# Performance work log

Measured on AMD Instinct MI355X. Metric: run time of the kernel, lower is better.

## Reference

```python
import jax, jax.numpy as jnp
import numpy as np

B, NTOK, NATOM = 2, 512, 16384
C_TOKEN, C_ATOM, C_PAIR, C_S = 384, 128, 16, 384
NQ, NK, H, NB = 32, 128, 4, 3
DH = C_ATOM // H
NW = NATOM // NQ


def _ln(x, g=None, b=None, eps=1e-5):
    mu = jnp.mean(x, -1, keepdims=True)
    var = jnp.mean((x - mu) ** 2, -1, keepdims=True)
    xn = (x - mu) * jax.lax.rsqrt(var + eps)
    if g is not None:
        xn = xn * g
    if b is not None:
        xn = xn + b
    return xn


def setup_inputs() -> dict:
    key = jax.random.key(0)
    ks = iter(jax.random.split(key, 64))
    def rn(shape, scale=1.0):
        return scale * jax.random.normal(next(ks), shape, jnp.float32)
    W = 0.02
    inp = {
        'a': rn((B, NTOK, C_TOKEN)),
        'r_l': rn((B, NATOM, 3)),
        'extra_feats': rn((B, NATOM, C_ATOM)),
        'p_lm': rn((B, NW, NQ, NK, C_PAIR)),
        'atom_mask': jnp.ones((B, NATOM), jnp.float32),
        'atom_to_token_idx': jnp.sort(jax.random.randint(next(ks), (B, NATOM), 0, NTOK, jnp.int32), axis=-1),
        # top-level params
        'Wa': rn((C_TOKEN, C_ATOM), W),
        'lnq_g': jnp.ones((C_ATOM,), jnp.float32),
        'lnq_b': jnp.zeros((C_ATOM,), jnp.float32),
        'Wout': rn((C_ATOM, 3), W),
        # per-block (stacked over NB) atom-transformer params
        'ag_w': rn((NB, C_S, C_ATOM), W), 'ag_b': jnp.zeros((NB, C_ATOM), jnp.float32),
        'ab_w': rn((NB, C_S, C_ATOM), W),
        'wq': rn((NB, C_ATOM, C_ATOM), W), 'bq': jnp.zeros((NB, C_ATOM), jnp.float32),
        'wk': rn((NB, C_ATOM, C_ATOM), W), 'wv': rn((NB, C_ATOM, C_ATOM), W),
        'pg': jnp.ones((NB, C_PAIR), jnp.float32), 'pb': jnp.zeros((NB, C_PAIR), jnp.float32),
        'wpb': rn((NB, C_PAIR, H), W),
        'wg': rn((NB, C_ATOM, C_ATOM), W), 'wo': rn((NB, C_ATOM, C_ATOM), W),
        'sk_w': rn((NB, C_S, C_ATOM), W), 'sk_b': jnp.full((NB, C_ATOM), -2.0, jnp.float32),
        'tg_w': rn((NB, C_S, C_ATOM), W), 'tg_b': jnp.zeros((NB, C_ATOM), jnp.float32),
        'tb_w': rn((NB, C_S, C_ATOM), W),
        'wt1': rn((NB, C_ATOM, 2 * C_ATOM), W), 'wt2': rn((NB, C_ATOM, 2 * C_ATOM), W),
        'wto': rn((NB, 2 * C_ATOM, C_ATOM), W),
        'tk_w': rn((NB, C_S, C_ATOM), W), 'tk_b': jnp.full((NB, C_ATOM), -2.0, jnp.float32),
    }
    return inp


def reference(a, r_l, extra_feats, p_lm, atom_mask, atom_to_token_idx,
              Wa, lnq_g, lnq_b, Wout,
              ag_w, ag_b, ab_w, wq, bq, wk, wv, pg, pb, wpb, wg, wo, sk_w, sk_b,
              tg_w, tg_b, tb_w, wt1, wt2, wto, tk_w, tk_b):
    # token -> atom broadcast
    q = a @ Wa                                                  # [B, NTOK, C_ATOM]
    q = jnp.take_along_axis(q, atom_to_token_idx[..., None], axis=1)  # [B, NATOM, C_ATOM]
    q = q + extra_feats
    am = atom_mask[..., None]
    q = q * am
    # conditioning signal: extra_feats zero-padded from C_ATOM to C_S (as in torch code)
    s = jnp.pad(extra_feats, ((0, 0), (0, 0), (0, C_S - C_ATOM)))
    sn = _ln(s)
    # sliding-window key indices: keys centered on each query window
    centers = jnp.arange(NW) * NQ + NQ // 2
    idx = (centers - NK // 2)[:, None] + jnp.arange(NK)          # [NW, NK]
    valid = ((idx >= 0) & (idx < NATOM)).astype(jnp.float32)
    idxc = jnp.clip(idx, 0, NATOM - 1)
    keymask = valid[None] * jnp.take(atom_mask, idxc, axis=1)    # [B, NW, NK]

    x = q
    inv_sqrt_dh = 1.0 / np.sqrt(DH)
    for i in range(NB):
        # --- attention with pair bias (AdaLN conditioned) ---
        xa = jax.nn.sigmoid(sn @ ag_w[i] + ag_b[i]) * _ln(x) + sn @ ab_w[i]
        qh = (xa @ wq[i] + bq[i]).reshape(B, NW, NQ, H, DH)
        kh = (xa @ wk[i]).reshape(B, NATOM, H, DH)
        vh = (xa @ wv[i]).reshape(B, NATOM, H, DH)
        kw = jnp.take(kh, idxc, axis=1)                          # [B, NW, NK, H, DH]
        vw = jnp.take(vh, idxc, axis=1)
        bias = _ln(p_lm, pg[i], pb[i]) @ wpb[i]                  # [B, NW, NQ, NK, H]
        scores = jnp.einsum('bwqhd,bwkhd->bwqkh', qh, kw) * inv_sqrt_dh + bias
        scores = jnp.where(keymask[:, :, None, :, None] > 0, scores, -1e9)
        attn = jax.nn.softmax(scores, axis=3)
        o = jnp.einsum('bwqkh,bwkhd->bwqhd', attn, vw).reshape(B, NATOM, C_ATOM)
        gate = jax.nn.sigmoid(xa @ wg[i])
        attn_out = (gate * o) @ wo[i]
        x = x + jax.nn.sigmoid(sn @ sk_w[i] + sk_b[i]) * attn_out
        # --- conditioned transition (SwiGLU) ---
        xt = jax.nn.sigmoid(sn @ tg_w[i] + tg_b[i]) * _ln(x) + sn @ tb_w[i]
        hsw = jax.nn.silu(xt @ wt1[i]) * (xt @ wt2[i])
        x = x + jax.nn.sigmoid(sn @ tk_w[i] + tk_b[i]) * (hsw @ wto[i])

    x = x * am
    r = _ln(x, lnq_g, lnq_b) @ Wout                              # [B, NATOM, 3]
    return r
```

## Files before the change

kernel.cpp:

```cpp
#include <hip/hip_runtime.h>
#include <hip/hip_bf16.h>

typedef __bf16 bf16;
typedef __bf16 bf16x8 __attribute__((ext_vector_type(8)));
typedef float f32x4 __attribute__((ext_vector_type(4)));

#define DEV static __device__ __forceinline__

#define BB 2
#define NTOK 512
#define NATOM 16384
#define CT 384
#define CA 128
#define CP 16
#define CS 384
#define NQ 32
#define NK 128
#define NH 4
#define DH 32
#define NWIN 512
#define MTOT (BB*NATOM)

DEV bf16x8 lds_ld8(const bf16* p){
  union { uint2 u[2]; bf16x8 v; } t;
  t.u[0] = *reinterpret_cast<const uint2*>(p);
  t.u[1] = *reinterpret_cast<const uint2*>(p + 4);
  return t.v;
}
DEV f32x4 mfma16(bf16x8 a, bf16x8 b, f32x4 c){
  return __builtin_amdgcn_mfma_f32_16x16x32_bf16(a, b, c, 0, 0, 0);
}
DEV float sigmoidf_(float x){ return 1.f/(1.f + __expf(-x)); }
DEV float red_sum64(float v){
  #pragma unroll
  for (int off = 1; off < 64; off <<= 1) v += __shfl_xor(v, off);
  return v;
}

DEV void stage_A64(const bf16* __restrict__ Ag, int ldA, int m0, int k0,
                   bf16 (*As)[72], int tid){
  #pragma unroll
  for (int i = 0; i < 2; i++){
    int c = tid + i*256;
    int row = c >> 3, off = (c & 7) * 8;
    uint4 d = *reinterpret_cast<const uint4*>(Ag + (size_t)(m0 + row)*ldA + k0 + off);
    uint2* dst = reinterpret_cast<uint2*>(&As[row][off]);
    dst[0] = make_uint2(d.x, d.y);
    dst[1] = make_uint2(d.z, d.w);
  }
}
DEV void stage_W64(const float* __restrict__ Wg, int ldW, int k0, int n0,
                   bf16 (*Ws)[72], int tid){
  #pragma unroll
  for (int i = 0; i < 4; i++){
    int c = tid + i*256;
    int row = c >> 4, off = (c & 15) * 4;
    float4 d = *reinterpret_cast<const float4*>(Wg + (size_t)(k0 + row)*ldW + n0 + off);
    Ws[off+0][row] = (bf16)d.x;
    Ws[off+1][row] = (bf16)d.y;
    Ws[off+2][row] = (bf16)d.z;
    Ws[off+3][row] = (bf16)d.w;
  }
}
DEV void mma64(const bf16 (*As)[72], const bf16 (*Ws)[72], int wave, int lane,
               f32x4 acc[2][2]){
  int wm = (wave >> 1) * 32, wn = (wave & 1) * 32;
  int l16 = lane & 15, q8 = (lane >> 4) * 8;
  #pragma unroll
  for (int ks = 0; ks < 2; ks++){
    bf16x8 a0 = lds_ld8(&As[wm + l16][ks*32 + q8]);
    bf16x8 a1 = lds_ld8(&As[wm + 16 + l16][ks*32 + q8]);
    bf16x8 b0 = lds_ld8(&Ws[wn + l16][ks*32 + q8]);
    bf16x8 b1 = lds_ld8(&Ws[wn + 16 + l16][ks*32 + q8]);
    acc[0][0] = mfma16(a0, b0, acc[0][0]);
    acc[0][1] = mfma16(a0, b1, acc[0][1]);
    acc[1][0] = mfma16(a1, b0, acc[1][0]);
    acc[1][1] = mfma16(a1, b1, acc[1][1]);
  }
}

__global__ __launch_bounds__(128) void token_gemm(const float* __restrict__ a,
    const float* __restrict__ Wa, float* __restrict__ aW){
  __shared__ float arow[CT];
  int row = blockIdx.x;
  for (int j = threadIdx.x; j < CT; j += 128) arow[j] = a[(size_t)row*CT + j];
  __syncthreads();
  int c = threadIdx.x;
  float s = 0.f;
  for (int j = 0; j < CT; j++) s += arow[j] * Wa[(size_t)j*CA + c];
  aW[(size_t)row*CA + c] = s;
}

__global__ __launch_bounds__(256) void build_x0(const float* __restrict__ aW,
    const float* __restrict__ ef, const float* __restrict__ amask,
    const int* __restrict__ a2t, float* __restrict__ x,
    bf16* __restrict__ snc, float* __restrict__ tval){
  int ga = blockIdx.x * 4 + (threadIdx.x >> 6);
  int lane = threadIdx.x & 63;
  int b = ga >> 14;
  int tok = a2t[ga];
  float2 av = *reinterpret_cast<const float2*>(aW + ((size_t)(b*NTOK + tok))*CA + lane*2);
  float2 ev = *reinterpret_cast<const float2*>(ef + (size_t)ga*CA + lane*2);
  float m = amask[ga];
  *reinterpret_cast<float2*>(x + (size_t)ga*CA + lane*2) =
      make_float2((av.x + ev.x)*m, (av.y + ev.y)*m);
  float s = red_sum64(ev.x + ev.y);
  float mu = s * (1.f/384.f);
  float d0 = ev.x - mu, d1 = ev.y - mu;
  float vs = red_sum64(d0*d0 + d1*d1);
  float var = (vs + 256.f*mu*mu) * (1.f/384.f);
  float rs = rsqrtf(var + 1e-5f);
  bf16* sp = snc + (size_t)ga*CA + lane*2;
  sp[0] = (bf16)(d0*rs); sp[1] = (bf16)(d1*rs);
  if (lane == 0) tval[ga] = -mu*rs;
}

__global__ __launch_bounds__(128) void colsums(const float* ag, const float* ab,
    const float* sk, const float* tg, const float* tb, const float* tk,
    float* __restrict__ cs){
  int mat = blockIdx.x;
  int i = mat / 6, t = mat % 6;
  const float* base = t==0?ag : t==1?ab : t==2?sk : t==3?tg : t==4?tb : tk;
  const float* W = base + (size_t)i*CS*CA;
  int c = threadIdx.x;
  float s = 0.f;
  for (int k = CA; k < CS; k++) s += W[(size_t)k*CA + c];
  cs[(size_t)mat*CA + c] = s;
}

__global__ __launch_bounds__(256) void cond_gemm(const bf16* __restrict__ snc,
    const float* __restrict__ tval,
    const float* ag, const float* ab, const float* sk,
    const float* tg, const float* tb, const float* tk,
    const float* agb, const float* skb, const float* tgb, const float* tkb,
    const float* __restrict__ cs, bf16* __restrict__ cond){
  __shared__ bf16 As[64][72];
  __shared__ bf16 Ws[64][72];
  int tid = threadIdx.x, wave = tid >> 6, lane = tid & 63;
  int m0 = blockIdx.x * 64, n0 = blockIdx.y * 64;
  int type = blockIdx.z;
  const float* W; const float* bias; int sig;
  switch (type){
    case 0:  W = ag; bias = agb;     sig = 1; break;
    case 1:  W = ab; bias = nullptr; sig = 0; break;
    case 2:  W = sk; bias = skb;     sig = 1; break;
    case 3:  W = tg; bias = tgb;     sig = 1; break;
    case 4:  W = tb; bias = nullptr; sig = 0; break;
    default: W = tk; bias = tkb;     sig = 1; break;
  }
  f32x4 z = {0.f,0.f,0.f,0.f};
  f32x4 acc[2][2] = {{z,z},{z,z}};
  for (int kt = 0; kt < CA; kt += 64){
    stage_A64(snc, CA, m0, kt, As, tid);
    stage_W64(W, CA, kt, n0, Ws, tid);
    __syncthreads();
    mma64(As, Ws, wave, lane, acc);
    __syncthreads();
  }
  int wm = (wave >> 1)*32, wn = (wave & 1)*32, l16 = lane & 15, quad = lane >> 4;
  const float* csrow = cs + (size_t)type*CA;
  bf16* outp = cond + (size_t)type*MTOT*CA;
  #pragma unroll
  for (int mt = 0; mt < 2; mt++)
  #pragma unroll
  for (int nt = 0; nt < 2; nt++)
  #pragma unroll
  for (int r = 0; r < 4; r++){
    int m = m0 + wm + mt*16 + quad*4 + r;
    int n = n0 + wn + nt*16 + l16;
    float v = acc[mt][nt][r] + tval[m]*csrow[n];
    if (bias) v += bias[n];
    if (sig)  v = sigmoidf_(v);
    outp[(size_t)m*CA + n] = (bf16)v;
  }
}

__global__ __launch_bounds__(256) void adaln_kernel(const float* __restrict__ x,
    const bf16* __restrict__ g, const bf16* __restrict__ bt, bf16* __restrict__ outp){
  int ga = blockIdx.x * 4 + (threadIdx.x >> 6);
  int lane = threadIdx.x & 63;
  float2 xv = *reinterpret_cast<const float2*>(x + (size_t)ga*CA + lane*2);
  float s = red_sum64(xv.x + xv.y);
  float mu = s * (1.f/128.f);
  float d0 = xv.x - mu, d1 = xv.y - mu;
  float vs = red_sum64(d0*d0 + d1*d1);
  float rs = rsqrtf(vs*(1.f/128.f) + 1e-5f);
  const bf16* gp = g  + (size_t)ga*CA + lane*2;
  const bf16* bp = bt + (size_t)ga*CA + lane*2;
  bf16* op = outp + (size_t)ga*CA + lane*2;
  op[0] = (bf16)((float)gp[0]*(d0*rs) + (float)bp[0]);
  op[1] = (bf16)((float)gp[1]*(d1*rs) + (float)bp[1]);
}

__global__ __launch_bounds__(256) void qkvg_gemm(const bf16* __restrict__ xa,
    const float* wq, const float* bq, const float* wk, const float* wv,
    const float* wg, bf16* __restrict__ outq){
  __shared__ bf16 As[64][72];
  __shared__ bf16 Ws[64][72];
  int tid = threadIdx.x, wave = tid >> 6, lane = tid & 63;
  int m0 = blockIdx.x * 64;
  int sel = blockIdx.y >> 1;
  int n0 = (blockIdx.y & 1) * 64;
  const float* W = sel==0 ? wq : sel==1 ? wk : sel==2 ? wv : wg;
  f32x4 z = {0.f,0.f,0.f,0.f};
  f32x4 acc[2][2] = {{z,z},{z,z}};
  for (int kt = 0; kt < CA; kt += 64){
    stage_A64(xa, CA, m0, kt, As, tid);
    stage_W64(W, CA, kt, n0, Ws, tid);
    __syncthreads();
    mma64(As, Ws, wave, lane, acc);
    __syncthreads();
  }
  int wm = (wave >> 1)*32, wn = (wave & 1)*32, l16 = lane & 15, quad = lane >> 4;
  #pragma unroll
  for (int mt = 0; mt < 2; mt++)
  #pragma unroll
  for (int nt = 0; nt < 2; nt++)
  #pragma unroll
  for (int r = 0; r < 4; r++){
    int m = m0 + wm + mt*16 + quad*4 + r;
    int n = n0 + wn + nt*16 + l16;
    float v = acc[mt][nt][r];
    if (sel == 0) v += bq[n];
    if (sel == 3) v = sigmoidf_(v);
    outq[(size_t)m*512 + sel*128 + n] = (bf16)v;
  }
}

__global__ __launch_bounds__(256) void attn_kernel(const bf16* __restrict__ qkvg,
    const float* __restrict__ p_lm, const float* __restrict__ amask,
    const float* __restrict__ pgv, const float* __restrict__ pbv,
    const float* __restrict__ wpbv, bf16* __restrict__ go){
  __shared__ bf16 Qs[32][136];
  __shared__ bf16 Ks[128][136];
  __shared__ bf16 Vts[128][136];
  __shared__ float kmask[128];
  int w = blockIdx.x, b = blockIdx.y;
  int tid = threadIdx.x;
  int wave = tid >> 6, lane = tid & 63, l16 = lane & 15, quad = lane >> 4;
  size_t abase = (size_t)b*NATOM + (size_t)w*NQ;
  int kstart = w*NQ + NQ/2 - NK/2;
  if (tid < 128){
    int pos = kstart + tid;
    kmask[tid] = (pos >= 0 && pos < NATOM) ? amask[(size_t)b*NATOM + pos] : 0.f;
  }
  #pragma unroll
  for (int i = 0; i < 2; i++){
    int c = tid + i*256;
    int row = c >> 4, off = (c & 15)*8;
    uint4 d = *reinterpret_cast<const uint4*>(qkvg + (abase + row)*512 + off);
    *reinterpret_cast<uint4*>(&Qs[row][off]) = d;
  }
  #pragma unroll
  for (int i = 0; i < 8; i++){
    int c = tid + i*256;
    int row = c >> 4, off = (c & 15)*8;
    int ka = kstart + row; ka = ka < 0 ? 0 : (ka > NATOM-1 ? NATOM-1 : ka);
    uint4 d = *reinterpret_cast<const uint4*>(qkvg + ((size_t)b*NATOM + ka)*512 + 128 + off);
    *reinterpret_cast<uint4*>(&Ks[row][off]) = d;
  }
  #pragma unroll
  for (int i = 0; i < 16; i++){
    int c = tid + i*256;
    int row = c >> 5, off = (c & 31)*4;
    int ka = kstart + row; ka = ka < 0 ? 0 : (ka > NATOM-1 ? NATOM-1 : ka);
    uint2 d = *reinterpret_cast<const uint2*>(qkvg + ((size_t)b*NATOM + ka)*512 + 256 + off);
    union { uint2 u; bf16 h[4]; } t; t.u = d;
    Vts[off+0][row] = t.h[0];
    Vts[off+1][row] = t.h[1];
    Vts[off+2][row] = t.h[2];
    Vts[off+3][row] = t.h[3];
  }
  __syncthreads();
  int h = wave;
  f32x4 z4 = {0.f,0.f,0.f,0.f};
  f32x4 sacc[2][8];
  #pragma unroll
  for (int mt = 0; mt < 2; mt++)
    #pragma unroll
    for (int nt = 0; nt < 8; nt++) sacc[mt][nt] = z4;
  {
    bf16x8 bfr[8];
    #pragma unroll
    for (int nt = 0; nt < 8; nt++) bfr[nt] = lds_ld8(&Ks[nt*16 + l16][h*32 + quad*8]);
    #pragma unroll
    for (int mt = 0; mt < 2; mt++){
      bf16x8 a = lds_ld8(&Qs[mt*16 + l16][h*32 + quad*8]);
      #pragma unroll
      for (int nt = 0; nt < 8; nt++) sacc[mt][nt] = mfma16(a, bfr[nt], sacc[mt][nt]);
    }
  }
  __syncthreads();
  f32x4 wj4[16]; f32x4 wsum4 = z4, cconst4 = z4;
  #pragma unroll
  for (int j = 0; j < 16; j++){
    f32x4 wp = { wpbv[j*4+0], wpbv[j*4+1], wpbv[j*4+2], wpbv[j*4+3] };
    wj4[j] = pgv[j] * wp;
    wsum4 += wj4[j];
    cconst4 += pbv[j] * wp;
  }
  size_t pbase = ((size_t)(b*NWIN + w)) * NQ * NK * CP;
  bf16* BiasBuf = &Ks[0][0];
  {
    #pragma unroll 4
    for (int t = 0; t < 16; t++){
      int pid = t*64 + lane;
      int q = pid >> 5;
      int k = wave*32 + (pid & 31);
      const float* pp = p_lm + pbase + ((size_t)q*NK + k)*CP;
      float4 p0 = *reinterpret_cast<const float4*>(pp);
      float4 p1 = *reinterpret_cast<const float4*>(pp + 4);
      float4 p2 = *reinterpret_cast<const float4*>(pp + 8);
      float4 p3 = *reinterpret_cast<const float4*>(pp + 12);
      float sm = p0.x+p0.y+p0.z+p0.w + p1.x+p1.y+p1.z+p1.w
               + p2.x+p2.y+p2.z+p2.w + p3.x+p3.y+p3.z+p3.w;
      float sq = p0.x*p0.x+p0.y*p0.y+p0.z*p0.z+p0.w*p0.w
               + p1.x*p1.x+p1.y*p1.y+p1.z*p1.z+p1.w*p1.w
               + p2.x*p2.x+p2.y*p2.y+p2.z*p2.z+p2.w*p2.w
               + p3.x*p3.x+p3.y*p3.y+p3.z*p3.z+p3.w*p3.w;
      f32x4 dw = z4;
      dw += p0.x*wj4[0];  dw += p0.y*wj4[1];  dw += p0.z*wj4[2];  dw += p0.w*wj4[3];
      dw += p1.x*wj4[4];  dw += p1.y*wj4[5];  dw += p1.z*wj4[6];  dw += p1.w*wj4[7];
      dw += p2.x*wj4[8];  dw += p2.y*wj4[9];  dw += p2.z*wj4[10]; dw += p2.w*wj4[11];
      dw += p3.x*wj4[12]; dw += p3.y*wj4[13]; dw += p3.z*wj4[14]; dw += p3.w*wj4[15];
      float mu = sm * (1.f/16.f);
      float var = fmaxf(sq*(1.f/16.f) - mu*mu, 0.f);
      float rsg = rsqrtf(var + 1e-5f);
      f32x4 bias4 = rsg*(dw - mu*wsum4) + cconst4;
      union { uint2 u; bf16 hh[4]; } tb;
      tb.hh[0] = (bf16)bias4.x; tb.hh[1] = (bf16)bias4.y;
      tb.hh[2] = (bf16)bias4.z; tb.hh[3] = (bf16)bias4.w;
      *reinterpret_cast<uint2*>(&BiasBuf[((size_t)q*NK + k)*4]) = tb.u;
    }
  }
  __syncthreads();
  const float invs = 0.17677669529663689f;
  #pragma unroll
  for (int mt = 0; mt < 2; mt++)
  #pragma unroll
  for (int r = 0; r < 4; r++){
    int q = mt*16 + quad*4 + r;
    #pragma unroll
    for (int nt = 0; nt < 8; nt++){
      int k = nt*16 + l16;
      float biasv = (float)BiasBuf[((size_t)q*NK + k)*4 + h];
      float sv = sacc[mt][nt][r]*invs + biasv;
      sacc[mt][nt][r] = (kmask[k] > 0.f) ? sv : -1e9f;
    }
  }
  float rinv[2][4];
  #pragma unroll
  for (int mt = 0; mt < 2; mt++)
  #pragma unroll
  for (int r = 0; r < 4; r++){
    float mx = -3.0e38f;
    #pragma unroll
    for (int nt = 0; nt < 8; nt++) mx = fmaxf(mx, sacc[mt][nt][r]);
    #pragma unroll
    for (int off = 1; off < 16; off <<= 1) mx = fmaxf(mx, __shfl_xor(mx, off));
    float ss = 0.f;
    #pragma unroll
    for (int nt = 0; nt < 8; nt++){
      float e = __expf(sacc[mt][nt][r] - mx);
      sacc[mt][nt][r] = e; ss += e;
    }
    #pragma unroll
    for (int off = 1; off < 16; off <<= 1) ss += __shfl_xor(ss, off);
    rinv[mt][r] = 1.f/ss;
  }
  __syncthreads();
  bf16 (*Ph)[136] = reinterpret_cast<bf16(*)[136]>(&Ks[h*32][0]);
  #pragma unroll
  for (int mt = 0; mt < 2; mt++)
  #pragma unroll
  for (int nt = 0; nt < 8; nt++)
  #pragma unroll
  for (int r = 0; r < 4; r++)
    Ph[mt*16 + quad*4 + r][nt*16 + l16] = (bf16)(sacc[mt][nt][r]*rinv[mt][r]);
  f32x4 oacc[2][2] = {{z4,z4},{z4,z4}};
  #pragma unroll
  for (int kt = 0; kt < 4; kt++){
    bf16x8 a0 = lds_ld8(&Ph[l16][kt*32 + quad*8]);
    bf16x8 a1 = lds_ld8(&Ph[16 + l16][kt*32 + quad*8]);
    bf16x8 b0 = lds_ld8(&Vts[h*32 + l16][kt*32 + quad*8]);
    bf16x8 b1 = lds_ld8(&Vts[h*32 + 16 + l16][kt*32 + quad*8]);
    oacc[0][0] = mfma16(a0, b0, oacc[0][0]);
    oacc[0][1] = mfma16(a0, b1, oacc[0][1]);
    oacc[1][0] = mfma16(a1, b0, oacc[1][0]);
    oacc[1][1] = mfma16(a1, b1, oacc[1][1]);
  }
  #pragma unroll
  for (int mt = 0; mt < 2; mt++)
  #pragma unroll
  for (int nt = 0; nt < 2; nt++)
  #pragma unroll
  for (int r = 0; r < 4; r++){
    int q = mt*16 + quad*4 + r;
    int dcol = h*32 + nt*16 + l16;
    size_t arow = abase + q;
    float gate = (float)qkvg[arow*512 + 384 + dcol];
    go[arow*CA + dcol] = (bf16)(gate * oacc[mt][nt][r]);
  }
}

template<int K>
__global__ __launch_bounds__(256) void resid_gemm(const bf16* __restrict__ Ain,
    const float* __restrict__ W, const bf16* __restrict__ gatec,
    float* __restrict__ x){
  __shared__ bf16 As[64][72];
  __shared__ bf16 Ws[64][72];
  int tid = threadIdx.x, wave = tid >> 6, lane = tid & 63;
  int m0 = blockIdx.x * 64, n0 = blockIdx.y * 64;
  f32x4 z = {0.f,0.f,0.f,0.f};
  f32x4 acc[2][2] = {{z,z},{z,z}};
  for (int kt = 0; kt < K; kt += 64){
    stage_A64(Ain, K, m0, kt, As, tid);
    stage_W64(W, CA, kt, n0, Ws, tid);
    __syncthreads();
    mma64(As, Ws, wave, lane, acc);
    __syncthreads();
  }
  int wm = (wave >> 1)*32, wn = (wave & 1)*32, l16 = lane & 15, quad = lane >> 4;
  #pragma unroll
  for (int mt = 0; mt < 2; mt++)
  #pragma unroll
  for (int nt = 0; nt < 2; nt++)
  #pragma unroll
  for (int r = 0; r < 4; r++){
    int m = m0 + wm + mt*16 + quad*4 + r;
    int n = n0 + wn + nt*16 + l16;
    size_t idx = (size_t)m*CA + n;
    x[idx] += (float)gatec[idx] * acc[mt][nt][r];
  }
}

__global__ __launch_bounds__(256) void t12_gemm(const bf16* __restrict__ xt,
    const float* __restrict__ w1, const float* __restrict__ w2,
    bf16* __restrict__ hsw){
  __shared__ bf16 As[64][72];
  __shared__ bf16 Ws[64][72];
  int tid = threadIdx.x, wave = tid >> 6, lane = tid & 63;
  int m0 = blockIdx.x * 64, n0 = blockIdx.y * 64;
  f32x4 z = {0.f,0.f,0.f,0.f};
  f32x4 acc1[2][2] = {{z,z},{z,z}};
  f32x4 acc2[2][2] = {{z,z},{z,z}};
  for (int kt = 0; kt < CA; kt += 64){
    stage_A64(xt, CA, m0, kt, As, tid);
    stage_W64(w1, 2*CA, kt, n0, Ws, tid);
    __syncthreads();
    mma64(As, Ws, wave, lane, acc1);
    __syncthreads();
    stage_W64(w2, 2*CA, kt, n0, Ws, tid);
    __syncthreads();
    mma64(As, Ws, wave, lane, acc2);
    __syncthreads();
  }
  int wm = (wave >> 1)*32, wn = (wave & 1)*32, l16 = lane & 15, quad = lane >> 4;
  #pragma unroll
  for (int mt = 0; mt < 2; mt++)
  #pragma unroll
  for (int nt = 0; nt < 2; nt++)
  #pragma unroll
  for (int r = 0; r < 4; r++){
    int m = m0 + wm + mt*16 + quad*4 + r;
    int n = n0 + wn + nt*16 + l16;
    float v1 = acc1[mt][nt][r];
    float v2 = acc2[mt][nt][r];
    hsw[(size_t)m*(2*CA) + n] = (bf16)(v1*sigmoidf_(v1)*v2);
  }
}

__global__ __launch_bounds__(256) void final_kernel(const float* __restrict__ x,
    const float* __restrict__ amask, const float* __restrict__ lg,
    const float* __restrict__ lb, const float* __restrict__ Wout,
    float* __restrict__ outp){
  int ga = blockIdx.x * 4 + (threadIdx.x >> 6);
  int lane = threadIdx.x & 63;
  float2 xv = *reinterpret_cast<const float2*>(x + (size_t)ga*CA + lane*2);
  float m = amask[ga];
  xv.x *= m; xv.y *= m;
  float s = red_sum64(xv.x + xv.y);
  float mu = s * (1.f/128.f);
  float d0 = xv.x - mu, d1 = xv.y - mu;
  float vs = red_sum64(d0*d0 + d1*d1);
  float rs = rsqrtf(vs*(1.f/128.f) + 1e-5f);
  int c = lane*2;
  float xn0 = d0*rs*lg[c]   + lb[c];
  float xn1 = d1*rs*lg[c+1] + lb[c+1];
  float p0 = xn0*Wout[c*3+0] + xn1*Wout[(c+1)*3+0];
  float p1 = xn0*Wout[c*3+1] + xn1*Wout[(c+1)*3+1];
  float p2 = xn0*Wout[c*3+2] + xn1*Wout[(c+1)*3+2];
  p0 = red_sum64(p0); p1 = red_sum64(p1); p2 = red_sum64(p2);
  if (lane == 0){
    outp[(size_t)ga*3 + 0] = p0;
    outp[(size_t)ga*3 + 1] = p1;
    outp[(size_t)ga*3 + 2] = p2;
  }
}

extern "C" void kernel_launch(void* const* d_in, const int* in_sizes, int n_in,
                              void* d_out, int out_size, void* d_ws, size_t ws_size,
                              hipStream_t stream){
  (void)in_sizes; (void)n_in; (void)out_size; (void)ws_size;
  const float* a     = (const float*)d_in[0];
  const float* ef    = (const float*)d_in[2];
  const float* p_lm  = (const float*)d_in[3];
  const float* amask = (const float*)d_in[4];
  const int*   a2t   = (const int*)d_in[5];
  const float* Wa    = (const float*)d_in[6];
  const float* lnq_g = (const float*)d_in[7];
  const float* lnq_b = (const float*)d_in[8];
  const float* Wout  = (const float*)d_in[9];
  const float* ag_w  = (const float*)d_in[10];
  const float* ag_b  = (const float*)d_in[11];
  const float* ab_w  = (const float*)d_in[12];
  const float* wq    = (const float*)d_in[13];
  const float* bq    = (const float*)d_in[14];
  const float* wk    = (const float*)d_in[15];
  const float* wv    = (const float*)d_in[16];
  const float* pg    = (const float*)d_in[17];
  const float* pb    = (const float*)d_in[18];
  const float* wpb   = (const float*)d_in[19];
  const float* wg    = (const float*)d_in[20];
  const float* wo    = (const float*)d_in[21];
  const float* sk_w  = (const float*)d_in[22];
  const float* sk_b  = (const float*)d_in[23];
  const float* tg_w  = (const float*)d_in[24];
  const float* tg_b  = (const float*)d_in[25];
  const float* tb_w  = (const float*)d_in[26];
  const float* wt1   = (const float*)d_in[27];
  const float* wt2   = (const float*)d_in[28];
  const float* wto   = (const float*)d_in[29];
  const float* tk_w  = (const float*)d_in[30];
  const float* tk_b  = (const float*)d_in[31];
  float* out = (float*)d_out;
  char* ws = (char*)d_ws;

  const size_t OFF_X    = 0;
  const size_t OFF_SNC  = OFF_X    + (size_t)MTOT*CA*4;
  const size_t OFF_TVAL = OFF_SNC  + (size_t)MTOT*CA*2;
  const size_t OFF_AW   = OFF_TVAL + (size_t)MTOT*4;
  const size_t OFF_CS   = OFF_AW   + (size_t)BB*NTOK*CA*4;
  const size_t OFF_COND = OFF_CS   + 18*CA*4 + 256;
  const size_t OFF_XA   = OFF_COND + (size_t)6*MTOT*CA*2;
  const size_t OFF_QKVG = OFF_XA   + (size_t)MTOT*CA*2;
  const size_t OFF_GO   = OFF_QKVG + (size_t)MTOT*512*2;

  float* x    = (float*)(ws + OFF_X);
  bf16*  snc  = (bf16*)(ws + OFF_SNC);
  float* tval = (float*)(ws + OFF_TVAL);
  float* aW   = (float*)(ws + OFF_AW);
  float* cs   = (float*)(ws + OFF_CS);
  bf16*  cond = (bf16*)(ws + OFF_COND);
  bf16*  xa   = (bf16*)(ws + OFF_XA);
  bf16*  qkvg = (bf16*)(ws + OFF_QKVG);
  bf16*  go   = (bf16*)(ws + OFF_GO);
  const size_t CSZ = (size_t)MTOT*CA;

  token_gemm<<<BB*NTOK, 128, 0, stream>>>(a, Wa, aW);
  build_x0<<<MTOT/4, 256, 0, stream>>>(aW, ef, amask, a2t, x, snc, tval);
  colsums<<<18, 128, 0, stream>>>(ag_w, ab_w, sk_w, tg_w, tb_w, tk_w, cs);

  for (int i = 0; i < 3; i++){
    size_t o384 = (size_t)i*CS*CA, o128 = (size_t)i*CA*CA, ob = (size_t)i*CA;
    cond_gemm<<<dim3(MTOT/64, 2, 6), 256, 0, stream>>>(snc, tval,
        ag_w + o384, ab_w + o384, sk_w + o384, tg_w + o384, tb_w + o384, tk_w + o384,
        ag_b + ob, sk_b + ob, tg_b + ob, tk_b + ob,
        cs + (size_t)i*6*CA, cond);
    adaln_kernel<<<MTOT/4, 256, 0, stream>>>(x, cond + 0*CSZ, cond + 1*CSZ, xa);
    qkvg_gemm<<<dim3(MTOT/64, 8), 256, 0, stream>>>(xa,
        wq + o128, bq + ob, wk + o128, wv + o128, wg + o128, qkvg);
    attn_kernel<<<dim3(NWIN, BB), 256, 0, stream>>>(qkvg, p_lm, amask,
        pg + (size_t)i*CP, pb + (size_t)i*CP, wpb + (size_t)i*CP*NH, go);
    resid_gemm<128><<<dim3(MTOT/64, 2), 256, 0, stream>>>(go, wo + o128,
        cond + 2*CSZ, x);
    adaln_kernel<<<MTOT/4, 256, 0, stream>>>(x, cond + 3*CSZ, cond + 4*CSZ, xa);
    t12_gemm<<<dim3(MTOT/64, 4), 256, 0, stream>>>(xa,
        wt1 + (size_t)i*CA*2*CA, wt2 + (size_t)i*CA*2*CA, qkvg );
    resid_gemm<256><<<dim3(MTOT/64, 2), 256, 0, stream>>>(qkvg ,
        wto + (size_t)i*2*CA*CA, cond + 5*CSZ, x);
  }
  final_kernel<<<MTOT/4, 256, 0, stream>>>(x, amask, lnq_g, lnq_b, Wout, out);
}
```

Measured before the change: 1.125 ms.

## Pre-convert weights to bf16, hoist bias/cond GEMMs, fuse residual with adaLN

Adds a one-time kernel that converts and transposes all weight matrices to bf16 [N][K] layout. The GEMMs then read A and B fragments straight from global memory into MFMA registers, with no LDS staging and no per-block fp32 conversion. The conditioning GEMMs for all three blocks run in one launch, and the pair-bias LayerNorm projection for all blocks is computed once up front and stored in bf16. The residual GEMMs now also apply the next adaLN, and the 1/sqrt(dh) scale is folded into Q. In exchange there are larger workspace buffers (18 cond tensors plus a precomputed bias tensor) and more global-memory traffic for B fragments with no LDS reuse.

```diff
diff --git a/kernel.cpp b/kernel.cpp
--- a/kernel.cpp
+++ b/kernel.cpp
@@ -20,6 +20,15 @@
 #define DH 32
 #define NWIN 512
 #define MTOT (BB*NATOM)
+#define CSZ ((size_t)MTOT*CA)
+
+#define WT_COND_OFF 0
+#define WT_QKVG_OFF 294912
+#define WT_WO_OFF   491520
+#define WT_T12_OFF  540672
+#define WT_WTO_OFF  737280
+#define WT_TOTAL    835584
+#define BIAS_I      16777216
 
 DEV bf16x8 lds_ld8(const bf16* p){
   union { uint2 u[2]; bf16x8 v; } t;
@@ -27,6 +36,11 @@
   t.u[1] = *reinterpret_cast<const uint2*>(p + 4);
   return t.v;
 }
+DEV bf16x8 ldg8(const bf16* p){
+  union { uint4 u; bf16x8 v; } t;
+  t.u = *reinterpret_cast<const uint4*>(p);
+  return t.v;
+}
 DEV f32x4 mfma16(bf16x8 a, bf16x8 b, f32x4 c){
   return __builtin_amdgcn_mfma_f32_16x16x32_bf16(a, b, c, 0, 0, 0);
 }
@@ -37,45 +51,46 @@
   return v;
 }
 
-DEV void stage_A64(const bf16* __restrict__ Ag, int ldA, int m0, int k0,
-                   bf16 (*As)[72], int tid){
-  #pragma unroll
-  for (int i = 0; i < 2; i++){
-    int c = tid + i*256;
-    int row = c >> 3, off = (c & 7) * 8;
-    uint4 d = *reinterpret_cast<const uint4*>(Ag + (size_t)(m0 + row)*ldA + k0 + off);
-    uint2* dst = reinterpret_cast<uint2*>(&As[row][off]);
-    dst[0] = make_uint2(d.x, d.y);
-    dst[1] = make_uint2(d.z, d.w);
-  }
-}
-DEV void stage_W64(const float* __restrict__ Wg, int ldW, int k0, int n0,
-                   bf16 (*Ws)[72], int tid){
-  #pragma unroll
-  for (int i = 0; i < 4; i++){
-    int c = tid + i*256;
-    int row = c >> 4, off = (c & 15) * 4;
-    float4 d = *reinterpret_cast<const float4*>(Wg + (size_t)(k0 + row)*ldW + n0 + off);
-    Ws[off+0][row] = (bf16)d.x;
-    Ws[off+1][row] = (bf16)d.y;
-    Ws[off+2][row] = (bf16)d.z;
-    Ws[off+3][row] = (bf16)d.w;
-  }
-}
-DEV void mma64(const bf16 (*As)[72], const bf16 (*Ws)[72], int wave, int lane,
-               f32x4 acc[2][2]){
-  int wm = (wave >> 1) * 32, wn = (wave & 1) * 32;
-  int l16 = lane & 15, q8 = (lane >> 4) * 8;
-  #pragma unroll
-  for (int ks = 0; ks < 2; ks++){
-    bf16x8 a0 = lds_ld8(&As[wm + l16][ks*32 + q8]);
-    bf16x8 a1 = lds_ld8(&As[wm + 16 + l16][ks*32 + q8]);
-    bf16x8 b0 = lds_ld8(&Ws[wn + l16][ks*32 + q8]);
-    bf16x8 b1 = lds_ld8(&Ws[wn + 16 + l16][ks*32 + q8]);
-    acc[0][0] = mfma16(a0, b0, acc[0][0]);
-    acc[0][1] = mfma16(a0, b1, acc[0][1]);
-    acc[1][0] = mfma16(a1, b0, acc[1][0]);
-    acc[1][1] = mfma16(a1, b1, acc[1][1]);
+__global__ __launch_bounds__(256) void wconv(
+    const float* ag, const float* ab, const float* sk,
+    const float* tg, const float* tb, const float* tk,
+    const float* wq, const float* wk, const float* wv, const float* wg,
+    const float* wo, const float* wt1, const float* wt2, const float* wto,
+    bf16* __restrict__ wt){
+  __shared__ __align__(16) bf16 T[64][264];
+  int s = blockIdx.x;
+  int mat, nslab;
+  if (s < 66){ mat = s >> 1; nslab = s & 1; }
+  else if (s < 90){ mat = 33 + (s-66)/4; nslab = (s-66)&3; }
+  else { mat = 39 + ((s-90)>>1); nslab = (s-90)&1; }
+  const float* src; int K, N; size_t dst;
+  if (mat < 18){ int i = mat/6, t = mat - i*6;
+    const float* base = t==0?ag:t==1?ab:t==2?sk:t==3?tg:t==4?tb:tk;
+    src = base + (size_t)i*CS*CA; K=128; N=128; dst = WT_COND_OFF + (size_t)mat*16384; }
+  else if (mat < 30){ int q = mat-18; int i=q>>2, sx=q&3;
+    const float* base = sx==0?wq:sx==1?wk:sx==2?wv:wg;
+    src = base + (size_t)i*16384; K=128; N=128; dst = WT_QKVG_OFF + (size_t)q*16384; }
+  else if (mat < 33){ src = wo + (size_t)(mat-30)*16384; K=128; N=128;
+    dst = WT_WO_OFF + (size_t)(mat-30)*16384; }
+  else if (mat < 39){ int q = mat-33; int i=q>>1, sx=q&1;
+    src = (sx? wt2 : wt1) + (size_t)i*32768; K=128; N=256;
+    dst = WT_T12_OFF + (size_t)q*32768; }
+  else { src = wto + (size_t)(mat-39)*32768; K=256; N=128;
+    dst = WT_WTO_OFF + (size_t)(mat-39)*32768; }
+  int n0 = nslab*64;
+  int tid = threadIdx.x;
+  for (int c = tid; c < K*16; c += 256){
+    int k = c >> 4, nq = c & 15;
+    float4 v = *reinterpret_cast<const float4*>(src + (size_t)k*N + n0 + nq*4);
+    T[nq*4+0][k] = (bf16)v.x; T[nq*4+1][k] = (bf16)v.y;
+    T[nq*4+2][k] = (bf16)v.z; T[nq*4+3][k] = (bf16)v.w;
+  }
+  __syncthreads();
+  int KQ = K >> 3;
+  for (int c = tid; c < 64*KQ; c += 256){
+    int n = c / KQ, kq = c - n*KQ;
+    uint4 d = *reinterpret_cast<const uint4*>(&T[n][kq*8]);
+    *reinterpret_cast<uint4*>(wt + dst + (size_t)(n0+n)*K + kq*8) = d;
   }
 }
 
@@ -128,50 +143,112 @@
   cs[(size_t)mat*CA + c] = s;
 }
 
-__global__ __launch_bounds__(256) void cond_gemm(const bf16* __restrict__ snc,
-    const float* __restrict__ tval,
-    const float* ag, const float* ab, const float* sk,
-    const float* tg, const float* tb, const float* tk,
-    const float* agb, const float* skb, const float* tgb, const float* tkb,
+__global__ __launch_bounds__(256) void cond_all(const bf16* __restrict__ snc,
+    const float* __restrict__ tval, const bf16* __restrict__ wtc,
+    const float* __restrict__ ag_b, const float* __restrict__ sk_b,
+    const float* __restrict__ tg_b, const float* __restrict__ tk_b,
     const float* __restrict__ cs, bf16* __restrict__ cond){
-  __shared__ bf16 As[64][72];
-  __shared__ bf16 Ws[64][72];
   int tid = threadIdx.x, wave = tid >> 6, lane = tid & 63;
-  int m0 = blockIdx.x * 64, n0 = blockIdx.y * 64;
-  int type = blockIdx.z;
-  const float* W; const float* bias; int sig;
-  switch (type){
-    case 0:  W = ag; bias = agb;     sig = 1; break;
-    case 1:  W = ab; bias = nullptr; sig = 0; break;
-    case 2:  W = sk; bias = skb;     sig = 1; break;
-    case 3:  W = tg; bias = tgb;     sig = 1; break;
-    case 4:  W = tb; bias = nullptr; sig = 0; break;
-    default: W = tk; bias = tkb;     sig = 1; break;
-  }
-  f32x4 z = {0.f,0.f,0.f,0.f};
-  f32x4 acc[2][2] = {{z,z},{z,z}};
-  for (int kt = 0; kt < CA; kt += 64){
-    stage_A64(snc, CA, m0, kt, As, tid);
-    stage_W64(W, CA, kt, n0, Ws, tid);
-    __syncthreads();
-    mma64(As, Ws, wave, lane, acc);
-    __syncthreads();
-  }
-  int wm = (wave >> 1)*32, wn = (wave & 1)*32, l16 = lane & 15, quad = lane >> 4;
-  const float* csrow = cs + (size_t)type*CA;
-  bf16* outp = cond + (size_t)type*MTOT*CA;
-  #pragma unroll
-  for (int mt = 0; mt < 2; mt++)
-  #pragma unroll
-  for (int nt = 0; nt < 2; nt++)
-  #pragma unroll
-  for (int r = 0; r < 4; r++){
-    int m = m0 + wm + mt*16 + quad*4 + r;
-    int n = n0 + wn + nt*16 + l16;
-    float v = acc[mt][nt][r] + tval[m]*csrow[n];
-    if (bias) v += bias[n];
-    if (sig)  v = sigmoidf_(v);
-    outp[(size_t)m*CA + n] = (bf16)v;
+  int l16 = lane & 15, quad = lane >> 4;
+  int m0 = blockIdx.x*64; int i = blockIdx.y;
+  const bf16* Ar = snc + (size_t)(m0 + wave*16 + l16)*CA;
+  bf16x8 a[4];
+  #pragma unroll
+  for (int ks = 0; ks < 4; ks++) a[ks] = ldg8(Ar + ks*32 + quad*8);
+  float tv[4];
+  #pragma unroll
+  for (int r = 0; r < 4; r++) tv[r] = tval[m0 + wave*16 + quad*4 + r];
+  for (int t = 0; t < 6; t++){
+    const bf16* Wt = wtc + (size_t)(i*6+t)*16384;
+    const float* csr = cs + (size_t)(i*6+t)*CA;
+    const float* bias = t==0 ? ag_b + (size_t)i*CA : t==2 ? sk_b + (size_t)i*CA
+                      : t==3 ? tg_b + (size_t)i*CA : t==5 ? tk_b + (size_t)i*CA : nullptr;
+    bool sig = (t==0)||(t==2)||(t==3)||(t==5);
+    f32x4 z = {0.f,0.f,0.f,0.f};
+    f32x4 acc[8];
+    #pragma unroll
+    for (int nt = 0; nt < 8; nt++) acc[nt] = z;
+    #pragma unroll
+    for (int nt = 0; nt < 8; nt++){
+      const bf16* Bp = Wt + (size_t)(nt*16 + l16)*128 + quad*8;
+      #pragma unroll
+      for (int ks = 0; ks < 4; ks++)
+        acc[nt] = mfma16(a[ks], ldg8(Bp + ks*32), acc[nt]);
+    }
+    bf16* op = cond + (size_t)(i*6+t)*CSZ;
+    #pragma unroll
+    for (int nt = 0; nt < 8; nt++)
+    #pragma unroll
+    for (int r = 0; r < 4; r++){
+      int m = m0 + wave*16 + quad*4 + r;
+      int n = nt*16 + l16;
+      float v = acc[nt][r] + tv[r]*csr[n];
+      if (bias) v += bias[n];
+      if (sig)  v = sigmoidf_(v);
+      op[(size_t)m*CA + n] = (bf16)v;
+    }
+  }
+}
+
+__global__ __launch_bounds__(256) void bias_all(const float* __restrict__ p_lm,
+    const float* __restrict__ pg, const float* __restrict__ pb,
+    const float* __restrict__ wpb, bf16* __restrict__ biasg){
+  __shared__ f32x4 wjS[3][16];
+  __shared__ f32x4 extraS[3][2];
+  int w = blockIdx.x, b = blockIdx.y;
+  int tid = threadIdx.x;
+  if (tid < 48){
+    int i = tid >> 4, j = tid & 15;
+    f32x4 wp = *reinterpret_cast<const f32x4*>(wpb + (size_t)(i*16+j)*4);
+    wjS[i][j] = pg[i*16+j]*wp;
+  }
+  __syncthreads();
+  if (tid < 3){
+    f32x4 s = {0.f,0.f,0.f,0.f}, c = {0.f,0.f,0.f,0.f};
+    for (int j = 0; j < 16; j++){
+      s += wjS[tid][j];
+      f32x4 wp = *reinterpret_cast<const f32x4*>(wpb + (size_t)(tid*16+j)*4);
+      c += pb[tid*16+j]*wp;
+    }
+    extraS[tid][0] = s; extraS[tid][1] = c;
+  }
+  __syncthreads();
+  size_t pbase = (size_t)(b*NWIN + w)*(NQ*NK*CP);
+  size_t obase = (size_t)(b*NWIN + w)*4096*4;
+  for (int i = 0; i < 3; i++){
+    f32x4 wj[16];
+    #pragma unroll
+    for (int j = 0; j < 16; j++) wj[j] = wjS[i][j];
+    f32x4 wsum = extraS[i][0], cc = extraS[i][1];
+    bf16* ob = biasg + (size_t)i*BIAS_I + obase;
+    #pragma unroll 2
+    for (int t = 0; t < 16; t++){
+      int pid = t*256 + tid;
+      const float* pp = p_lm + pbase + (size_t)pid*16;
+      float4 p0 = *reinterpret_cast<const float4*>(pp);
+      float4 p1 = *reinterpret_cast<const float4*>(pp + 4);
+      float4 p2 = *reinterpret_cast<const float4*>(pp + 8);
+      float4 p3 = *reinterpret_cast<const float4*>(pp + 12);
+      float sm = p0.x+p0.y+p0.z+p0.w + p1.x+p1.y+p1.z+p1.w
+               + p2.x+p2.y+p2.z+p2.w + p3.x+p3.y+p3.z+p3.w;
+      float sq = p0.x*p0.x+p0.y*p0.y+p0.z*p0.z+p0.w*p0.w
+               + p1.x*p1.x+p1.y*p1.y+p1.z*p1.z+p1.w*p1.w
+               + p2.x*p2.x+p2.y*p2.y+p2.z*p2.z+p2.w*p2.w
+               + p3.x*p3.x+p3.y*p3.y+p3.z*p3.z+p3.w*p3.w;
+      f32x4 dw = {0.f,0.f,0.f,0.f};
+      dw += p0.x*wj[0];  dw += p0.y*wj[1];  dw += p0.z*wj[2];  dw += p0.w*wj[3];
+      dw += p1.x*wj[4];  dw += p1.y*wj[5];  dw += p1.z*wj[6];  dw += p1.w*wj[7];
+      dw += p2.x*wj[8];  dw += p2.y*wj[9];  dw += p2.z*wj[10]; dw += p2.w*wj[11];
+      dw += p3.x*wj[12]; dw += p3.y*wj[13]; dw += p3.z*wj[14]; dw += p3.w*wj[15];
+      float mu = sm * (1.f/16.f);
+      float var = fmaxf(sq*(1.f/16.f) - mu*mu, 0.f);
+      float rsg = rsqrtf(var + 1e-5f);
+      f32x4 b4 = rsg*(dw - mu*wsum) + cc;
+      union { uint2 u; bf16 hh[4]; } tb;
+      tb.hh[0] = (bf16)b4.x; tb.hh[1] = (bf16)b4.y;
+      tb.hh[2] = (bf16)b4.z; tb.hh[3] = (bf16)b4.w;
+      *reinterpret_cast<uint2*>(ob + (size_t)pid*4) = tb.u;
+    }
   }
 }
 
@@ -193,44 +270,45 @@
 }
 
 __global__ __launch_bounds__(256) void qkvg_gemm(const bf16* __restrict__ xa,
-    const float* wq, const float* bq, const float* wk, const float* wv,
-    const float* wg, bf16* __restrict__ outq){
-  __shared__ bf16 As[64][72];
-  __shared__ bf16 Ws[64][72];
+    const bf16* __restrict__ wt, const float* __restrict__ bq,
+    bf16* __restrict__ outq){
   int tid = threadIdx.x, wave = tid >> 6, lane = tid & 63;
-  int m0 = blockIdx.x * 64;
-  int sel = blockIdx.y >> 1;
-  int n0 = (blockIdx.y & 1) * 64;
-  const float* W = sel==0 ? wq : sel==1 ? wk : sel==2 ? wv : wg;
+  int l16 = lane & 15, quad = lane >> 4;
+  int m0 = blockIdx.x*64;
+  int sel = blockIdx.y;
+  const bf16* Wt = wt + (size_t)sel*16384;
+  const bf16* Ar = xa + (size_t)(m0 + wave*16 + l16)*CA;
+  bf16x8 a[4];
+  #pragma unroll
+  for (int ks = 0; ks < 4; ks++) a[ks] = ldg8(Ar + ks*32 + quad*8);
   f32x4 z = {0.f,0.f,0.f,0.f};
-  f32x4 acc[2][2] = {{z,z},{z,z}};
-  for (int kt = 0; kt < CA; kt += 64){
-    stage_A64(xa, CA, m0, kt, As, tid);
-    stage_W64(W, CA, kt, n0, Ws, tid);
-    __syncthreads();
-    mma64(As, Ws, wave, lane, acc);
-    __syncthreads();
-  }
-  int wm = (wave >> 1)*32, wn = (wave & 1)*32, l16 = lane & 15, quad = lane >> 4;
-  #pragma unroll
-  for (int mt = 0; mt < 2; mt++)
-  #pragma unroll
-  for (int nt = 0; nt < 2; nt++)
+  f32x4 acc[8];
+  #pragma unroll
+  for (int nt = 0; nt < 8; nt++) acc[nt] = z;
+  #pragma unroll
+  for (int nt = 0; nt < 8; nt++){
+    const bf16* Bp = Wt + (size_t)(nt*16 + l16)*128 + quad*8;
+    #pragma unroll
+    for (int ks = 0; ks < 4; ks++)
+      acc[nt] = mfma16(a[ks], ldg8(Bp + ks*32), acc[nt]);
+  }
+  const float invs = 0.17677669529663689f;
+  #pragma unroll
+  for (int nt = 0; nt < 8; nt++)
   #pragma unroll
   for (int r = 0; r < 4; r++){
-    int m = m0 + wm + mt*16 + quad*4 + r;
-    int n = n0 + wn + nt*16 + l16;
-    float v = acc[mt][nt][r];
-    if (sel == 0) v += bq[n];
+    int m = m0 + wave*16 + quad*4 + r;
+    int n = nt*16 + l16;
+    float v = acc[nt][r];
+    if (sel == 0) v = (v + bq[n]) * invs;
     if (sel == 3) v = sigmoidf_(v);
     outq[(size_t)m*512 + sel*128 + n] = (bf16)v;
   }
 }
 
 __global__ __launch_bounds__(256) void attn_kernel(const bf16* __restrict__ qkvg,
-    const float* __restrict__ p_lm, const float* __restrict__ amask,
-    const float* __restrict__ pgv, const float* __restrict__ pbv,
-    const float* __restrict__ wpbv, bf16* __restrict__ go){
+    const bf16* __restrict__ biasg, const float* __restrict__ amask,
+    bf16* __restrict__ go){
   __shared__ bf16 Qs[32][136];
   __shared__ bf16 Ks[128][136];
   __shared__ bf16 Vts[128][136];
@@ -290,51 +368,7 @@
       for (int nt = 0; nt < 8; nt++) sacc[mt][nt] = mfma16(a, bfr[nt], sacc[mt][nt]);
     }
   }
-  __syncthreads();
-  f32x4 wj4[16]; f32x4 wsum4 = z4, cconst4 = z4;
-  #pragma unroll
-  for (int j = 0; j < 16; j++){
-    f32x4 wp = { wpbv[j*4+0], wpbv[j*4+1], wpbv[j*4+2], wpbv[j*4+3] };
-    wj4[j] = pgv[j] * wp;
-    wsum4 += wj4[j];
-    cconst4 += pbv[j] * wp;
-  }
-  size_t pbase = ((size_t)(b*NWIN + w)) * NQ * NK * CP;
-  bf16* BiasBuf = &Ks[0][0];
-  {
-    #pragma unroll 4
-    for (int t = 0; t < 16; t++){
-      int pid = t*64 + lane;
-      int q = pid >> 5;
-      int k = wave*32 + (pid & 31);
-      const float* pp = p_lm + pbase + ((size_t)q*NK + k)*CP;
-      float4 p0 = *reinterpret_cast<const float4*>(pp);
-      float4 p1 = *reinterpret_cast<const float4*>(pp + 4);
-      float4 p2 = *reinterpret_cast<const float4*>(pp + 8);
-      float4 p3 = *reinterpret_cast<const float4*>(pp + 12);
-      float sm = p0.x+p0.y+p0.z+p0.w + p1.x+p1.y+p1.z+p1.w
-               + p2.x+p2.y+p2.z+p2.w + p3.x+p3.y+p3.z+p3.w;
-      float sq = p0.x*p0.x+p0.y*p0.y+p0.z*p0.z+p0.w*p0.w
-               + p1.x*p1.x+p1.y*p1.y+p1.z*p1.z+p1.w*p1.w
-               + p2.x*p2.x+p2.y*p2.y+p2.z*p2.z+p2.w*p2.w
-               + p3.x*p3.x+p3.y*p3.y+p3.z*p3.z+p3.w*p3.w;
-      f32x4 dw = z4;
-      dw += p0.x*wj4[0];  dw += p0.y*wj4[1];  dw += p0.z*wj4[2];  dw += p0.w*wj4[3];
-      dw += p1.x*wj4[4];  dw += p1.y*wj4[5];  dw += p1.z*wj4[6];  dw += p1.w*wj4[7];
-      dw += p2.x*wj4[8];  dw += p2.y*wj4[9];  dw += p2.z*wj4[10]; dw += p2.w*wj4[11];
-      dw += p3.x*wj4[12]; dw += p3.y*wj4[13]; dw += p3.z*wj4[14]; dw += p3.w*wj4[15];
-      float mu = sm * (1.f/16.f);
-      float var = fmaxf(sq*(1.f/16.f) - mu*mu, 0.f);
-      float rsg = rsqrtf(var + 1e-5f);
-      f32x4 bias4 = rsg*(dw - mu*wsum4) + cconst4;
-      union { uint2 u; bf16 hh[4]; } tb;
-      tb.hh[0] = (bf16)bias4.x; tb.hh[1] = (bf16)bias4.y;
-      tb.hh[2] = (bf16)bias4.z; tb.hh[3] = (bf16)bias4.w;
-      *reinterpret_cast<uint2*>(&BiasBuf[((size_t)q*NK + k)*4]) = tb.u;
-    }
-  }
-  __syncthreads();
-  const float invs = 0.17677669529663689f;
+  const bf16* bp = biasg + ((size_t)(b*NWIN + w)*4096)*4;
   #pragma unroll
   for (int mt = 0; mt < 2; mt++)
   #pragma unroll
@@ -343,8 +377,8 @@
     #pragma unroll
     for (int nt = 0; nt < 8; nt++){
       int k = nt*16 + l16;
-      float biasv = (float)BiasBuf[((size_t)q*NK + k)*4 + h];
-      float sv = sacc[mt][nt][r]*invs + biasv;
+      float biasv = (float)bp[((size_t)q*128 + k)*4 + h];
+      float sv = sacc[mt][nt][r] + biasv;
       sacc[mt][nt][r] = (kmask[k] > 0.f) ? sv : -1e9f;
     }
   }
@@ -403,69 +437,101 @@
   }
 }
 
-template<int K>
-__global__ __launch_bounds__(256) void resid_gemm(const bf16* __restrict__ Ain,
-    const float* __restrict__ W, const bf16* __restrict__ gatec,
-    float* __restrict__ x){
-  __shared__ bf16 As[64][72];
-  __shared__ bf16 Ws[64][72];
+template<int K, bool FUSE>
+__global__ __launch_bounds__(256) void resid_fused(const bf16* __restrict__ Ain,
+    const bf16* __restrict__ Wt, const bf16* __restrict__ gsk,
+    float* __restrict__ x,
+    const bf16* __restrict__ lng, const bf16* __restrict__ lnb,
+    bf16* __restrict__ xaout){
+  constexpr int KT = K/32;
   int tid = threadIdx.x, wave = tid >> 6, lane = tid & 63;
-  int m0 = blockIdx.x * 64, n0 = blockIdx.y * 64;
+  int l16 = lane & 15, quad = lane >> 4;
+  int m0 = blockIdx.x*64;
+  const bf16* Ar = Ain + (size_t)(m0 + wave*16 + l16)*K;
+  bf16x8 a[KT];
+  #pragma unroll
+  for (int ks = 0; ks < KT; ks++) a[ks] = ldg8(Ar + ks*32 + quad*8);
   f32x4 z = {0.f,0.f,0.f,0.f};
-  f32x4 acc[2][2] = {{z,z},{z,z}};
-  for (int kt = 0; kt < K; kt += 64){
-    stage_A64(Ain, K, m0, kt, As, tid);
-    stage_W64(W, CA, kt, n0, Ws, tid);
-    __syncthreads();
-    mma64(As, Ws, wave, lane, acc);
-    __syncthreads();
-  }
-  int wm = (wave >> 1)*32, wn = (wave & 1)*32, l16 = lane & 15, quad = lane >> 4;
-  #pragma unroll
-  for (int mt = 0; mt < 2; mt++)
-  #pragma unroll
-  for (int nt = 0; nt < 2; nt++)
+  f32x4 acc[8];
+  #pragma unroll
+  for (int nt = 0; nt < 8; nt++) acc[nt] = z;
+  #pragma unroll
+  for (int nt = 0; nt < 8; nt++){
+    const bf16* Bp = Wt + (size_t)(nt*16 + l16)*K + quad*8;
+    #pragma unroll
+    for (int ks = 0; ks < KT; ks++)
+      acc[nt] = mfma16(a[ks], ldg8(Bp + ks*32), acc[nt]);
+  }
+  int mrow = m0 + wave*16 + quad*4;
+  #pragma unroll
+  for (int nt = 0; nt < 8; nt++)
   #pragma unroll
   for (int r = 0; r < 4; r++){
-    int m = m0 + wm + mt*16 + quad*4 + r;
-    int n = n0 + wn + nt*16 + l16;
-    size_t idx = (size_t)m*CA + n;
-    x[idx] += (float)gatec[idx] * acc[mt][nt][r];
+    size_t idx = (size_t)(mrow + r)*CA + nt*16 + l16;
+    float v = x[idx] + (float)gsk[idx]*acc[nt][r];
+    x[idx] = v;
+    acc[nt][r] = v;
+  }
+  if constexpr (FUSE){
+    #pragma unroll
+    for (int r = 0; r < 4; r++){
+      float s = 0.f;
+      #pragma unroll
+      for (int nt = 0; nt < 8; nt++) s += acc[nt][r];
+      #pragma unroll
+      for (int off = 1; off < 16; off <<= 1) s += __shfl_xor(s, off);
+      float mu = s*(1.f/128.f);
+      float vs = 0.f;
+      #pragma unroll
+      for (int nt = 0; nt < 8; nt++){
+        float d = acc[nt][r] - mu; vs += d*d;
+      }
+      #pragma unroll
+      for (int off = 1; off < 16; off <<= 1) vs += __shfl_xor(vs, off);
+      float rs = rsqrtf(vs*(1.f/128.f) + 1e-5f);
+      #pragma unroll
+      for (int nt = 0; nt < 8; nt++){
+        size_t idx = (size_t)(mrow + r)*CA + nt*16 + l16;
+        float xn = (acc[nt][r] - mu)*rs;
+        xaout[idx] = (bf16)((float)lng[idx]*xn + (float)lnb[idx]);
+      }
+    }
   }
 }
 
 __global__ __launch_bounds__(256) void t12_gemm(const bf16* __restrict__ xt,
-    const float* __restrict__ w1, const float* __restrict__ w2,
+    const bf16* __restrict__ Wt1, const bf16* __restrict__ Wt2,
     bf16* __restrict__ hsw){
-  __shared__ bf16 As[64][72];
-  __shared__ bf16 Ws[64][72];
   int tid = threadIdx.x, wave = tid >> 6, lane = tid & 63;
-  int m0 = blockIdx.x * 64, n0 = blockIdx.y * 64;
+  int l16 = lane & 15, quad = lane >> 4;
+  int m0 = blockIdx.x*64;
+  int n0 = blockIdx.y*128;
+  const bf16* Ar = xt + (size_t)(m0 + wave*16 + l16)*CA;
+  bf16x8 a[4];
+  #pragma unroll
+  for (int ks = 0; ks < 4; ks++) a[ks] = ldg8(Ar + ks*32 + quad*8);
   f32x4 z = {0.f,0.f,0.f,0.f};
-  f32x4 acc1[2][2] = {{z,z},{z,z}};
-  f32x4 acc2[2][2] = {{z,z},{z,z}};
-  for (int kt = 0; kt < CA; kt += 64){
-    stage_A64(xt, CA, m0, kt, As, tid);
-    stage_W64(w1, 2*CA, kt, n0, Ws, tid);
-    __syncthreads();
-    mma64(As, Ws, wave, lane, acc1);
-    __syncthreads();
-    stage_W64(w2, 2*CA, kt, n0, Ws, tid);
-    __syncthreads();
-    mma64(As, Ws, wave, lane, acc2);
-    __syncthreads();
-  }
-  int wm = (wave >> 1)*32, wn = (wave & 1)*32, l16 = lane & 15, quad = lane >> 4;
-  #pragma unroll
-  for (int mt = 0; mt < 2; mt++)
-  #pragma unroll
-  for (int nt = 0; nt < 2; nt++)
+  f32x4 acc1[8], acc2[8];
+  #pragma unroll
+  for (int nt = 0; nt < 8; nt++){ acc1[nt] = z; acc2[nt] = z; }
+  #pragma unroll
+  for (int nt = 0; nt < 8; nt++){
+    const bf16* Bp1 = Wt1 + (size_t)(n0 + nt*16 + l16)*128 + quad*8;
+    const bf16* Bp2 = Wt2 + (size_t)(n0 + nt*16 + l16)*128 + quad*8;
+    #pragma unroll
+    for (int ks = 0; ks < 4; ks++){
+      acc1[nt] = mfma16(a[ks], ldg8(Bp1 + ks*32), acc1[nt]);
+      acc2[nt] = mfma16(a[ks], ldg8(Bp2 + ks*32), acc2[nt]);
+    }
+  }
+  #pragma unroll
+  for (int nt = 0; nt < 8; nt++)
   #pragma unroll
   for (int r = 0; r < 4; r++){
-    int m = m0 + wm + mt*16 + quad*4 + r;
-    int n = n0 + wn + nt*16 + l16;
-    float v1 = acc1[mt][nt][r];
-    float v2 = acc2[mt][nt][r];
+    int m = m0 + wave*16 + quad*4 + r;
+    int n = n0 + nt*16 + l16;
+    float v1 = acc1[nt][r];
+    float v2 = acc2[nt][r];
     hsw[(size_t)m*(2*CA) + n] = (bf16)(v1*sigmoidf_(v1)*v2);
   }
 }
@@ -541,44 +607,56 @@
   const size_t OFF_TVAL = OFF_SNC  + (size_t)MTOT*CA*2;
   const size_t OFF_AW   = OFF_TVAL + (size_t)MTOT*4;
   const size_t OFF_CS   = OFF_AW   + (size_t)BB*NTOK*CA*4;
-  const size_t OFF_COND = OFF_CS   + 18*CA*4 + 256;
-  const size_t OFF_XA   = OFF_COND + (size_t)6*MTOT*CA*2;
+  const size_t OFF_WT   = OFF_CS   + 18*CA*4 + 256;
+  const size_t OFF_COND = OFF_WT   + (size_t)WT_TOTAL*2 + 256;
+  const size_t OFF_XA   = OFF_COND + (size_t)18*CSZ*2;
   const size_t OFF_QKVG = OFF_XA   + (size_t)MTOT*CA*2;
-  const size_t OFF_GO   = OFF_QKVG + (size_t)MTOT*512*2;
+  const size_t OFF_HSW  = OFF_QKVG + (size_t)MTOT*512*2;
+  const size_t OFF_GO   = OFF_HSW  + (size_t)MTOT*256*2;
+  const size_t OFF_BIAS = OFF_GO   + (size_t)MTOT*CA*2;
 
   float* x    = (float*)(ws + OFF_X);
   bf16*  snc  = (bf16*)(ws + OFF_SNC);
   float* tval = (float*)(ws + OFF_TVAL);
   float* aW   = (float*)(ws + OFF_AW);
   float* cs   = (float*)(ws + OFF_CS);
+  bf16*  wt   = (bf16*)(ws + OFF_WT);
   bf16*  cond = (bf16*)(ws + OFF_COND);
   bf16*  xa   = (bf16*)(ws + OFF_XA);
   bf16*  qkvg = (bf16*)(ws + OFF_QKVG);
+  bf16*  hsw  = (bf16*)(ws + OFF_HSW);
   bf16*  go   = (bf16*)(ws + OFF_GO);
-  const size_t CSZ = (size_t)MTOT*CA;
+  bf16*  biasg= (bf16*)(ws + OFF_BIAS);
 
   token_gemm<<<BB*NTOK, 128, 0, stream>>>(a, Wa, aW);
   build_x0<<<MTOT/4, 256, 0, stream>>>(aW, ef, amask, a2t, x, snc, tval);
+  wconv<<<96, 256, 0, stream>>>(ag_w, ab_w, sk_w, tg_w, tb_w, tk_w,
+      wq, wk, wv, wg, wo, wt1, wt2, wto, wt);
   colsums<<<18, 128, 0, stream>>>(ag_w, ab_w, sk_w, tg_w, tb_w, tk_w, cs);
+  cond_all<<<dim3(MTOT/64, 3), 256, 0, stream>>>(snc, tval, wt + WT_COND_OFF,
+      ag_b, sk_b, tg_b, tk_b, cs, cond);
+  bias_all<<<dim3(NWIN, BB), 256, 0, stream>>>(p_lm, pg, pb, wpb, biasg);
+  adaln_kernel<<<MTOT/4, 256, 0, stream>>>(x, cond, cond + CSZ, xa);
 
   for (int i = 0; i < 3; i++){
-    size_t o384 = (size_t)i*CS*CA, o128 = (size_t)i*CA*CA, ob = (size_t)i*CA;
-    cond_gemm<<<dim3(MTOT/64, 2, 6), 256, 0, stream>>>(snc, tval,
-        ag_w + o384, ab_w + o384, sk_w + o384, tg_w + o384, tb_w + o384, tk_w + o384,
-        ag_b + ob, sk_b + ob, tg_b + ob, tk_b + ob,
-        cs + (size_t)i*6*CA, cond);
-    adaln_kernel<<<MTOT/4, 256, 0, stream>>>(x, cond + 0*CSZ, cond + 1*CSZ, xa);
-    qkvg_gemm<<<dim3(MTOT/64, 8), 256, 0, stream>>>(xa,
-        wq + o128, bq + ob, wk + o128, wv + o128, wg + o128, qkvg);
-    attn_kernel<<<dim3(NWIN, BB), 256, 0, stream>>>(qkvg, p_lm, amask,
-        pg + (size_t)i*CP, pb + (size_t)i*CP, wpb + (size_t)i*CP*NH, go);
-    resid_gemm<128><<<dim3(MTOT/64, 2), 256, 0, stream>>>(go, wo + o128,
-        cond + 2*CSZ, x);
-    adaln_kernel<<<MTOT/4, 256, 0, stream>>>(x, cond + 3*CSZ, cond + 4*CSZ, xa);
-    t12_gemm<<<dim3(MTOT/64, 4), 256, 0, stream>>>(xa,
-        wt1 + (size_t)i*CA*2*CA, wt2 + (size_t)i*CA*2*CA, qkvg );
-    resid_gemm<256><<<dim3(MTOT/64, 2), 256, 0, stream>>>(qkvg ,
-        wto + (size_t)i*2*CA*CA, cond + 5*CSZ, x);
+    qkvg_gemm<<<dim3(MTOT/64, 4), 256, 0, stream>>>(xa,
+        wt + WT_QKVG_OFF + (size_t)i*4*16384, bq + (size_t)i*CA, qkvg);
+    attn_kernel<<<dim3(NWIN, BB), 256, 0, stream>>>(qkvg,
+        biasg + (size_t)i*BIAS_I, amask, go);
+    resid_fused<128,true><<<MTOT/64, 256, 0, stream>>>(go,
+        wt + WT_WO_OFF + (size_t)i*16384, cond + (size_t)(i*6+2)*CSZ, x,
+        cond + (size_t)(i*6+3)*CSZ, cond + (size_t)(i*6+4)*CSZ, xa);
+    t12_gemm<<<dim3(MTOT/64, 2), 256, 0, stream>>>(xa,
+        wt + WT_T12_OFF + (size_t)(2*i)*32768,
+        wt + WT_T12_OFF + (size_t)(2*i+1)*32768, hsw);
+    if (i < 2)
+      resid_fused<256,true><<<MTOT/64, 256, 0, stream>>>(hsw,
+          wt + WT_WTO_OFF + (size_t)i*32768, cond + (size_t)(i*6+5)*CSZ, x,
+          cond + (size_t)((i+1)*6+0)*CSZ, cond + (size_t)((i+1)*6+1)*CSZ, xa);
+    else
+      resid_fused<256,false><<<MTOT/64, 256, 0, stream>>>(hsw,
+          wt + WT_WTO_OFF + (size_t)i*32768, cond + (size_t)(i*6+5)*CSZ, x,
+          nullptr, nullptr, nullptr);
   }
   final_kernel<<<MTOT/4, 256, 0, stream>>>(x, amask, lnq_g, lnq_b, Wout, out);
 }
```

After: 1.278 ms. 1.14x slower.
